# Kernel optimization log

Measured on AMD Instinct MI355X. Metric: run time of the kernel, lower is better.

## Reference

```python
import jax, jax.numpy as jnp
import numpy as np

D_MODEL = 1024
NUM_HEADS = 16
HEAD_DIM = D_MODEL // NUM_HEADS
B, S = 2, 2048


def setup_inputs() -> dict:
    key = jax.random.key(0)
    ks = jax.random.split(key, 16)
    sd = 1.0 / np.sqrt(D_MODEL)
    def lin(k):
        kw, kb = jax.random.split(k)
        W = jax.random.uniform(kw, (D_MODEL, D_MODEL), jnp.float32, -sd, sd)
        b = jax.random.uniform(kb, (D_MODEL,), jnp.float32, -sd, sd)
        return W, b
    Wq, bq = lin(ks[0]); Wk, bk = lin(ks[1]); Wv, bv = lin(ks[2]); Wo, bo = lin(ks[3])
    return {
        'q': jax.random.normal(ks[4], (B, S, D_MODEL), jnp.float32),
        'k': jax.random.normal(ks[5], (B, S, D_MODEL), jnp.float32),
        'v': jax.random.normal(ks[6], (B, S, D_MODEL), jnp.float32),
        'phase': jax.random.normal(ks[7], (B,), jnp.float32),
        'Wq': Wq, 'bq': bq, 'Wk': Wk, 'bk': bk, 'Wv': Wv, 'bv': bv, 'Wo': Wo, 'bo': bo,
        'phase_coupling': jnp.zeros((1, NUM_HEADS, 1, 1), jnp.float32),
        'attention_scale': jnp.ones((1,), jnp.float32),
        'stability_factor': jnp.ones((1,), jnp.float32),
    }


def reference(q, k, v, phase, Wq, bq, Wk, bk, Wv, bv, Wo, bo,
              phase_coupling, attention_scale, stability_factor):
    batch, seq, _ = q.shape
    scale = HEAD_DIM ** -0.5

    def split_heads(x):  # [B,S,D] -> [B,H,S,hd]
        return x.reshape(batch, -1, NUM_HEADS, HEAD_DIM).transpose(0, 2, 1, 3)

    qh = split_heads(q @ Wq.T + bq)
    kh = split_heads(k @ Wk.T + bk)
    vh = split_heads(v @ Wv.T + bv)

    scores = jnp.einsum('bhqd,bhkd->bhqk', qh, kh) * (scale * attention_scale)
    # phase modulation: phase [B] -> [B,1,1,1]; scores *= 1 + coupling*sin(phase)
    phase_factor = jnp.sin(phase)[:, None, None, None]
    scores = scores * (1.0 + phase_coupling * phase_factor)

    attn_weights = jax.nn.softmax(scores, axis=-1)  # dropout is identity in eval
    out = jnp.einsum('bhqk,bhkd->bhqd', attn_weights, vh)
    out = out.transpose(0, 2, 1, 3).reshape(batch, seq, D_MODEL)
    out = (out @ Wo.T + bo) * stability_factor
    return out, attn_weights
```

## Files before the change

kernel.cpp:

```cpp
#include <hip/hip_runtime.h>
#include <hip/hip_bf16.h>
#include <cstdint>
#include <cstddef>
#include <cmath>

#define NH 16
#define HD 64
#define SS 2048
#define DM 1024
#define MTOT 4096

typedef __attribute__((ext_vector_type(8))) short short8;
typedef __attribute__((ext_vector_type(4))) float float4v;
typedef __attribute__((ext_vector_type(4))) int int4v;
typedef __attribute__((ext_vector_type(4))) unsigned short ushort4v;

__device__ __forceinline__ unsigned short f2bf(float f){
  unsigned int u = __builtin_bit_cast(unsigned int, f);
  u += 0x7FFFu + ((u >> 16) & 1u);
  return (unsigned short)(u >> 16);
}

__device__ __forceinline__ void gload16(const void* g, void* l){
  __builtin_amdgcn_global_load_lds((const __attribute__((address_space(1))) void*)g,
                                   (__attribute__((address_space(3))) void*)l, 16, 0, 0);
}

__global__ __launch_bounds__(256) void cvt3_kernel(
    const float* __restrict__ s0, const float* __restrict__ s1, const float* __restrict__ s2,
    unsigned short* __restrict__ d0, unsigned short* __restrict__ d1, unsigned short* __restrict__ d2,
    int n){
  const int z = blockIdx.z;
  const float* src = z==0 ? s0 : (z==1 ? s1 : s2);
  unsigned short* dst = z==0 ? d0 : (z==1 ? d1 : d2);
  for (int i = (blockIdx.x*blockDim.x + threadIdx.x)*4; i < n; i += gridDim.x*blockDim.x*4){
    float4v v = *reinterpret_cast<const float4v*>(src + i);
    ushort4v o;
    o.x = f2bf(v.x); o.y = f2bf(v.y); o.z = f2bf(v.z); o.w = f2bf(v.w);
    *reinterpret_cast<ushort4v*>(dst + i) = o;
  }
}

__global__ __launch_bounds__(256) void cvt4_kernel(
    const float* __restrict__ s0, const float* __restrict__ s1,
    const float* __restrict__ s2, const float* __restrict__ s3,
    unsigned short* __restrict__ d0, unsigned short* __restrict__ d1,
    unsigned short* __restrict__ d2, unsigned short* __restrict__ d3,
    int n){
  const int z = blockIdx.z;
  const float* src = z==0 ? s0 : (z==1 ? s1 : (z==2 ? s2 : s3));
  unsigned short* dst = z==0 ? d0 : (z==1 ? d1 : (z==2 ? d2 : d3));
  for (int i = (blockIdx.x*blockDim.x + threadIdx.x)*4; i < n; i += gridDim.x*blockDim.x*4){
    float4v v = *reinterpret_cast<const float4v*>(src + i);
    ushort4v o;
    o.x = f2bf(v.x); o.y = f2bf(v.y); o.z = f2bf(v.z); o.w = f2bf(v.w);
    *reinterpret_cast<ushort4v*>(dst + i) = o;
  }
}

__global__ __launch_bounds__(256) void gemm_proj(
    const unsigned short* __restrict__ X0, const unsigned short* __restrict__ X1, const unsigned short* __restrict__ X2,
    const unsigned short* __restrict__ W0, const unsigned short* __restrict__ W1, const unsigned short* __restrict__ W2,
    const float* __restrict__ b0, const float* __restrict__ b1, const float* __restrict__ b2,
    unsigned short* __restrict__ O0, unsigned short* __restrict__ O1, unsigned short* __restrict__ O2){
  __shared__ unsigned short Alds[128*32];
  __shared__ unsigned short Blds[128*32];
  const int z = blockIdx.z;
  const unsigned short* A  = z==0 ? X0 : (z==1 ? X1 : X2);
  const unsigned short* Bw = z==0 ? W0 : (z==1 ? W1 : W2);
  const float* bias        = z==0 ? b0 : (z==1 ? b1 : b2);
  unsigned short* outp     = z==0 ? O0 : (z==1 ? O1 : O2);
  const bool vmode = (z == 2);
  const int K = DM;
  const int t = threadIdx.x;
  const int l = t & 63;
  const int w = t >> 6;
  const int m0 = blockIdx.y * 128, n0 = blockIdx.x * 128;
  const int wm = (w & 1)*64, wn = (w >> 1)*64;
  const int srow = t >> 2;
  const int scol = (t & 3)*8;
  const int lr = l & 15, lg = l >> 4;
  float4v acc[4][4] = {};
  for (int k0 = 0; k0 < K; k0 += 32){
    __syncthreads();
    gload16(A  + (size_t)(m0 + srow     )*K + k0 + scol, Alds + t*8);
    gload16(A  + (size_t)(m0 + srow + 64)*K + k0 + scol, Alds + 2048 + t*8);
    gload16(Bw + (size_t)(n0 + srow     )*K + k0 + scol, Blds + t*8);
    gload16(Bw + (size_t)(n0 + srow + 64)*K + k0 + scol, Blds + 2048 + t*8);
    asm volatile("s_waitcnt vmcnt(0)" ::: "memory");
    __syncthreads();
    short8 afrag[4], bfrag[4];
    #pragma unroll
    for (int mb = 0; mb < 4; ++mb)
      afrag[mb] = *reinterpret_cast<const short8*>(Alds + (wm + mb*16 + lr)*32 + lg*8);
    #pragma unroll
    for (int nb = 0; nb < 4; ++nb)
      bfrag[nb] = *reinterpret_cast<const short8*>(Blds + (wn + nb*16 + lr)*32 + lg*8);
    #pragma unroll
    for (int mb = 0; mb < 4; ++mb)
      #pragma unroll
      for (int nb = 0; nb < 4; ++nb)
        acc[mb][nb] = __builtin_amdgcn_mfma_f32_16x16x32_bf16(afrag[mb], bfrag[nb], acc[mb][nb], 0, 0, 0);
  }
  #pragma unroll
  for (int mb = 0; mb < 4; ++mb){
    #pragma unroll
    for (int nb = 0; nb < 4; ++nb){
      const int gn = n0 + wn + nb*16 + lr;
      const float biasv = bias[gn];
      #pragma unroll
      for (int r = 0; r < 4; ++r){
        const int gm = m0 + wm + mb*16 + lg*4 + r;
        float v = acc[mb][nb][r] + biasv;
        const int b_ = gm >> 11, s_ = gm & 2047, h_ = gn >> 6, d_ = gn & 63;
        if (!vmode)
          outp[((size_t)(b_*NH + h_)*SS + s_)*HD + d_] = f2bf(v);
        else
          outp[((size_t)(b_*NH + h_)*HD + d_)*SS + s_] = f2bf(v);
      }
    }
  }
}

__global__ __launch_bounds__(256) void gemm_out(const unsigned short* __restrict__ A,
                                                const unsigned short* __restrict__ Bw,
                                                const float* __restrict__ bias,
                                                float* __restrict__ outp,
                                                const float* __restrict__ oscale_p){
  __shared__ unsigned short Alds[128*32];
  __shared__ unsigned short Blds[128*32];
  const int K = DM, N = DM;
  const int t = threadIdx.x;
  const int l = t & 63;
  const int w = t >> 6;
  const int m0 = blockIdx.y * 128, n0 = blockIdx.x * 128;
  const int wm = (w & 1)*64, wn = (w >> 1)*64;
  const int srow = t >> 2;
  const int scol = (t & 3)*8;
  const int lr = l & 15, lg = l >> 4;
  float4v acc[4][4] = {};
  for (int k0 = 0; k0 < K; k0 += 32){
    __syncthreads();
    gload16(A  + (size_t)(m0 + srow     )*K + k0 + scol, Alds + t*8);
    gload16(A  + (size_t)(m0 + srow + 64)*K + k0 + scol, Alds + 2048 + t*8);
    gload16(Bw + (size_t)(n0 + srow     )*K + k0 + scol, Blds + t*8);
    gload16(Bw + (size_t)(n0 + srow + 64)*K + k0 + scol, Blds + 2048 + t*8);
    asm volatile("s_waitcnt vmcnt(0)" ::: "memory");
    __syncthreads();
    short8 afrag[4], bfrag[4];
    #pragma unroll
    for (int mb = 0; mb < 4; ++mb)
      afrag[mb] = *reinterpret_cast<const short8*>(Alds + (wm + mb*16 + lr)*32 + lg*8);
    #pragma unroll
    for (int nb = 0; nb < 4; ++nb)
      bfrag[nb] = *reinterpret_cast<const short8*>(Blds + (wn + nb*16 + lr)*32 + lg*8);
    #pragma unroll
    for (int mb = 0; mb < 4; ++mb)
      #pragma unroll
      for (int nb = 0; nb < 4; ++nb)
        acc[mb][nb] = __builtin_amdgcn_mfma_f32_16x16x32_bf16(afrag[mb], bfrag[nb], acc[mb][nb], 0, 0, 0);
  }
  const float osc = oscale_p[0];
  #pragma unroll
  for (int mb = 0; mb < 4; ++mb){
    #pragma unroll
    for (int nb = 0; nb < 4; ++nb){
      const int gn = n0 + wn + nb*16 + lr;
      const float biasv = bias[gn];
      #pragma unroll
      for (int r = 0; r < 4; ++r){
        const int gm = m0 + wm + mb*16 + lg*4 + r;
        outp[(size_t)gm*N + gn] = (acc[mb][nb][r] + biasv) * osc;
      }
    }
  }
}

__global__ __launch_bounds__(256, 4) void attn_kernel(
    const unsigned short* __restrict__ Qh,
    const unsigned short* __restrict__ Kh,
    const unsigned short* __restrict__ Vt,
    unsigned short* __restrict__ AO,
    float* __restrict__ attnW,
    const float* __restrict__ phase,
    const float* __restrict__ pc,
    const float* __restrict__ ascale)
{
  __shared__ float lred[4][32];
  __shared__ __attribute__((aligned(16))) float ored[4][32*32];

  const int t = threadIdx.x;
  const int w = t >> 6, l = t & 63;
  const int lr = l & 15, lg = l >> 4;
  const int bh = blockIdx.x, qt = blockIdx.y;
  const int b = bh >> 4, h = bh & 15;
  const int q0 = qt*32;
  const float scale2 = 0.125f * ascale[0] * (1.0f + pc[h] * sinf(phase[b]))
                       * 1.4426950408889634f;

  const unsigned short* qbase = Qh + ((size_t)bh*SS + q0 + lr)*HD + lg*8;
  short8 aq[2][2];
  aq[0][0] = *reinterpret_cast<const short8*>(qbase);
  aq[0][1] = *reinterpret_cast<const short8*>(qbase + 32);
  aq[1][0] = *reinterpret_cast<const short8*>(qbase + 16*HD);
  aq[1][1] = *reinterpret_cast<const short8*>(qbase + 16*HD + 32);

  const int tbase = w * 512;
  const unsigned short* kbase = Kh + ((size_t)bh*SS + tbase + lr)*HD + lg*8;

  float lsum[2] = {0.f, 0.f};
  #pragma unroll 2
  for (int tb = 0; tb < 32; ++tb){
    const unsigned short* kp = kbase + (size_t)tb*16*HD;
    short8 bk0 = *reinterpret_cast<const short8*>(kp);
    short8 bk1 = *reinterpret_cast<const short8*>(kp + 32);
    #pragma unroll
    for (int qs = 0; qs < 2; ++qs){
      float4v pacc = {};
      pacc = __builtin_amdgcn_mfma_f32_16x16x32_bf16(bk0, aq[qs][0], pacc, 0, 0, 0);
      pacc = __builtin_amdgcn_mfma_f32_16x16x32_bf16(bk1, aq[qs][1], pacc, 0, 0, 0);
      lsum[qs] += (exp2f(pacc[0]*scale2) + exp2f(pacc[1]*scale2))
                + (exp2f(pacc[2]*scale2) + exp2f(pacc[3]*scale2));
    }
  }
  #pragma unroll
  for (int mask = 16; mask < 64; mask <<= 1){
    lsum[0] += __shfl_xor(lsum[0], mask, 64);
    lsum[1] += __shfl_xor(lsum[1], mask, 64);
  }
  if (l < 16){
    lred[w][lr]    = lsum[0];
    lred[w][16+lr] = lsum[1];
  }
  __syncthreads();
  float cc[2];
  #pragma unroll
  for (int qs = 0; qs < 2; ++qs){
    const int row = qs*16 + lr;
    const float total = (lred[0][row] + lred[1][row]) + (lred[2][row] + lred[3][row]);
    cc[qs] = -__log2f(total);
  }

  float4v oacc[2][4] = {};
  float* gwq0 = attnW + ((size_t)bh*SS + q0 + lr)*SS + tbase;
  float* gwq1 = gwq0 + (size_t)16*SS;
  const unsigned short* vbase = Vt + ((size_t)bh*HD + lr)*SS + tbase + lg*8;
  const int idxA = (((lg & 1)*2)*16 + lr)*4;
  const int idxB = idxA + 64;
  const bool hi = (lg >= 2);

  short8 cA0 = *reinterpret_cast<const short8*>(kbase);
  short8 cA1 = *reinterpret_cast<const short8*>(kbase + 32);
  short8 cB0 = *reinterpret_cast<const short8*>(kbase + 16*HD);
  short8 cB1 = *reinterpret_cast<const short8*>(kbase + 16*HD + 32);
  short8 cv0 = *reinterpret_cast<const short8*>(vbase);
  short8 cv1 = *reinterpret_cast<const short8*>(vbase + (size_t)16*SS);
  short8 cv2 = *reinterpret_cast<const short8*>(vbase + (size_t)32*SS);
  short8 cv3 = *reinterpret_cast<const short8*>(vbase + (size_t)48*SS);

  #pragma unroll 2
  for (int tp = 0; tp < 16; ++tp){
    const int tn = (tp + 1) & 15;
    const unsigned short* kpn = kbase + (size_t)tn*32*HD;
    const short8 nA0 = *reinterpret_cast<const short8*>(kpn);
    const short8 nA1 = *reinterpret_cast<const short8*>(kpn + 32);
    const short8 nB0 = *reinterpret_cast<const short8*>(kpn + 16*HD);
    const short8 nB1 = *reinterpret_cast<const short8*>(kpn + 16*HD + 32);
    const short8 nv0 = *reinterpret_cast<const short8*>(vbase + tn*32);
    const short8 nv1 = *reinterpret_cast<const short8*>(vbase + (size_t)16*SS + tn*32);
    const short8 nv2 = *reinterpret_cast<const short8*>(vbase + (size_t)32*SS + tn*32);
    const short8 nv3 = *reinterpret_cast<const short8*>(vbase + (size_t)48*SS + tn*32);

    const int tloc = tp*32;
    #pragma unroll
    for (int qs = 0; qs < 2; ++qs){
      float4v pA = {};
      pA = __builtin_amdgcn_mfma_f32_16x16x32_bf16(cA0, aq[qs][0], pA, 0, 0, 0);
      pA = __builtin_amdgcn_mfma_f32_16x16x32_bf16(cA1, aq[qs][1], pA, 0, 0, 0);
      float4v pB = {};
      pB = __builtin_amdgcn_mfma_f32_16x16x32_bf16(cB0, aq[qs][0], pB, 0, 0, 0);
      pB = __builtin_amdgcn_mfma_f32_16x16x32_bf16(cB1, aq[qs][1], pB, 0, 0, 0);
      float4v eA, eB;
      eA.x = exp2f(fmaf(pA[0], scale2, cc[qs]));
      eA.y = exp2f(fmaf(pA[1], scale2, cc[qs]));
      eA.z = exp2f(fmaf(pA[2], scale2, cc[qs]));
      eA.w = exp2f(fmaf(pA[3], scale2, cc[qs]));
      eB.x = exp2f(fmaf(pB[0], scale2, cc[qs]));
      eB.y = exp2f(fmaf(pB[1], scale2, cc[qs]));
      eB.z = exp2f(fmaf(pB[2], scale2, cc[qs]));
      eB.w = exp2f(fmaf(pB[3], scale2, cc[qs]));
      const int w0A = ((int)f2bf(eA.y) << 16) | (int)f2bf(eA.x);
      const int w1A = ((int)f2bf(eA.w) << 16) | (int)f2bf(eA.z);
      const int w0B = ((int)f2bf(eB.y) << 16) | (int)f2bf(eB.x);
      const int w1B = ((int)f2bf(eB.w) << 16) | (int)f2bf(eB.z);

      const int a0 = __builtin_amdgcn_ds_bpermute(idxA, w0A);
      const int b0 = __builtin_amdgcn_ds_bpermute(idxA, w0B);
      const int a1 = __builtin_amdgcn_ds_bpermute(idxA, w1A);
      const int b1 = __builtin_amdgcn_ds_bpermute(idxA, w1B);
      const int a2 = __builtin_amdgcn_ds_bpermute(idxB, w0A);
      const int b2 = __builtin_amdgcn_ds_bpermute(idxB, w0B);
      const int a3 = __builtin_amdgcn_ds_bpermute(idxB, w1A);
      const int b3 = __builtin_amdgcn_ds_bpermute(idxB, w1B);
      int4v words;
      words.x = hi ? b0 : a0;
      words.y = hi ? b1 : a1;
      words.z = hi ? b2 : a2;
      words.w = hi ? b3 : a3;
      const short8 pa = __builtin_bit_cast(short8, words);

      oacc[qs][0] = __builtin_amdgcn_mfma_f32_16x16x32_bf16(pa, cv0, oacc[qs][0], 0, 0, 0);
      oacc[qs][1] = __builtin_amdgcn_mfma_f32_16x16x32_bf16(pa, cv1, oacc[qs][1], 0, 0, 0);
      oacc[qs][2] = __builtin_amdgcn_mfma_f32_16x16x32_bf16(pa, cv2, oacc[qs][2], 0, 0, 0);
      oacc[qs][3] = __builtin_amdgcn_mfma_f32_16x16x32_bf16(pa, cv3, oacc[qs][3], 0, 0, 0);

      float* gw = qs ? gwq1 : gwq0;
      __builtin_nontemporal_store(eA, reinterpret_cast<float4v*>(gw + tloc + lg*4));
      __builtin_nontemporal_store(eB, reinterpret_cast<float4v*>(gw + tloc + 16 + lg*4));
    }

    cA0 = nA0; cA1 = nA1; cB0 = nB0; cB1 = nB1;
    cv0 = nv0; cv1 = nv1; cv2 = nv2; cv3 = nv3;
  }

  #pragma unroll
  for (int c = 0; c < 2; ++c){
    if (c) __syncthreads();
    #pragma unroll
    for (int qs = 0; qs < 2; ++qs)
      #pragma unroll
      for (int dl = 0; dl < 2; ++dl)
        #pragma unroll
        for (int r = 0; r < 4; ++r)
          ored[w][(qs*16 + lg*4 + r)*32 + dl*16 + lr] = oacc[qs][c*2 + dl][r];
    __syncthreads();
    const int row = t >> 3, c4 = (t & 7);
    const float4v* o0 = reinterpret_cast<const float4v*>(&ored[0][0]);
    const int fi = row*8 + c4;
    float4v s = o0[fi];
    s += o0[fi + 256];
    s += o0[fi + 512];
    s += o0[fi + 768];
    ushort4v o4;
    o4.x = f2bf(s.x); o4.y = f2bf(s.y); o4.z = f2bf(s.z); o4.w = f2bf(s.w);
    *reinterpret_cast<ushort4v*>(AO + ((size_t)b*SS + q0 + row)*DM + h*HD + c*32 + c4*4) = o4;
  }
}

extern "C" void kernel_launch(void* const* d_in, const int* in_sizes, int n_in,
                              void* d_out, int out_size, void* d_ws, size_t ws_size,
                              hipStream_t stream){
  const float* q      = (const float*)d_in[0];
  const float* k      = (const float*)d_in[1];
  const float* v      = (const float*)d_in[2];
  const float* phase  = (const float*)d_in[3];
  const float* Wq     = (const float*)d_in[4];
  const float* bq     = (const float*)d_in[5];
  const float* Wk     = (const float*)d_in[6];
  const float* bk     = (const float*)d_in[7];
  const float* Wv     = (const float*)d_in[8];
  const float* bv     = (const float*)d_in[9];
  const float* Wo     = (const float*)d_in[10];
  const float* bo     = (const float*)d_in[11];
  const float* pc     = (const float*)d_in[12];
  const float* ascale = (const float*)d_in[13];
  const float* stab   = (const float*)d_in[14];

  unsigned short* Xq  = (unsigned short*)d_ws;
  unsigned short* Xk  = Xq  + 4194304;
  unsigned short* Xv  = Xk  + 4194304;
  unsigned short* Wqb = Xv  + 4194304;
  unsigned short* Wkb = Wqb + 1048576;
  unsigned short* Wvb = Wkb + 1048576;
  unsigned short* Wob = Wvb + 1048576;
  unsigned short* Qh  = Wob + 1048576;
  unsigned short* Kh  = Qh  + 4194304;
  unsigned short* Vt  = Kh  + 4194304;
  unsigned short* AO  = Vt  + 4194304;

  float* out0  = (float*)d_out;
  float* attnW = out0 + (size_t)MTOT*DM;

  cvt3_kernel<<<dim3(512,1,3), 256, 0, stream>>>(q, k, v, Xq, Xk, Xv, MTOT*DM);
  cvt4_kernel<<<dim3(128,1,4), 256, 0, stream>>>(Wq, Wk, Wv, Wo, Wqb, Wkb, Wvb, Wob, DM*DM);

  gemm_proj<<<dim3(DM/128, MTOT/128, 3), 256, 0, stream>>>(
      Xq, Xk, Xv, Wqb, Wkb, Wvb, bq, bk, bv, Qh, Kh, Vt);

  attn_kernel<<<dim3(32, SS/32, 1), 256, 0, stream>>>(Qh, Kh, Vt, AO, attnW,
                                                      phase, pc, ascale);

  gemm_out<<<dim3(DM/128, MTOT/128, 1), 256, 0, stream>>>(AO, Wob, bo, out0, stab);
}
```

Baseline: 310.3 us.

## Stage attention-weight tiles in LDS for coalesced full-row global stores

The second pass of the attention kernel now walks the keys in chunks of 256, with the four waves interleaved inside each chunk. The exp-normalized weights are written to a padded shared-memory tile and then stored to the attention-weight output as contiguous 1 KB row segments, replacing the scattered 16-byte nontemporal stores. The aim is better write coalescing for the large fp32 attention-weight output. The cost is two block barriers per chunk, extra LDS traffic and a larger shared footprint (about 33 KB), and the register prefetch of the next K/V tiles has been removed.

```diff
diff --git a/kernel.cpp b/kernel.cpp
--- a/kernel.cpp
+++ b/kernel.cpp
@@ -187,7 +187,7 @@
     const float* __restrict__ ascale)
 {
   __shared__ float lred[4][32];
-  __shared__ __attribute__((aligned(16))) float ored[4][32*32];
+  __shared__ __attribute__((aligned(16))) float smem[32*260];
 
   const int t = threadIdx.x;
   const int w = t >> 6, l = t & 63;
@@ -205,13 +205,11 @@
   aq[1][0] = *reinterpret_cast<const short8*>(qbase + 16*HD);
   aq[1][1] = *reinterpret_cast<const short8*>(qbase + 16*HD + 32);
 
-  const int tbase = w * 512;
-  const unsigned short* kbase = Kh + ((size_t)bh*SS + tbase + lr)*HD + lg*8;
-
+  const unsigned short* kbase1 = Kh + ((size_t)bh*SS + w*512 + lr)*HD + lg*8;
   float lsum[2] = {0.f, 0.f};
   #pragma unroll 2
   for (int tb = 0; tb < 32; ++tb){
-    const unsigned short* kp = kbase + (size_t)tb*16*HD;
+    const unsigned short* kp = kbase1 + (size_t)tb*16*HD;
     short8 bk0 = *reinterpret_cast<const short8*>(kp);
     short8 bk1 = *reinterpret_cast<const short8*>(kp + 32);
     #pragma unroll
@@ -242,87 +240,84 @@
   }
 
   float4v oacc[2][4] = {};
-  float* gwq0 = attnW + ((size_t)bh*SS + q0 + lr)*SS + tbase;
-  float* gwq1 = gwq0 + (size_t)16*SS;
-  const unsigned short* vbase = Vt + ((size_t)bh*HD + lr)*SS + tbase + lg*8;
+  float* gwb = attnW + ((size_t)bh*SS + q0)*SS;
+  const unsigned short* kb2 = Kh + ((size_t)bh*SS + lr)*HD + lg*8;
+  const unsigned short* vb2 = Vt + ((size_t)bh*HD + lr)*SS + lg*8;
   const int idxA = (((lg & 1)*2)*16 + lr)*4;
   const int idxB = idxA + 64;
   const bool hi = (lg >= 2);
 
-  short8 cA0 = *reinterpret_cast<const short8*>(kbase);
-  short8 cA1 = *reinterpret_cast<const short8*>(kbase + 32);
-  short8 cB0 = *reinterpret_cast<const short8*>(kbase + 16*HD);
-  short8 cB1 = *reinterpret_cast<const short8*>(kbase + 16*HD + 32);
-  short8 cv0 = *reinterpret_cast<const short8*>(vbase);
-  short8 cv1 = *reinterpret_cast<const short8*>(vbase + (size_t)16*SS);
-  short8 cv2 = *reinterpret_cast<const short8*>(vbase + (size_t)32*SS);
-  short8 cv3 = *reinterpret_cast<const short8*>(vbase + (size_t)48*SS);
-
-  #pragma unroll 2
-  for (int tp = 0; tp < 16; ++tp){
-    const int tn = (tp + 1) & 15;
-    const unsigned short* kpn = kbase + (size_t)tn*32*HD;
-    const short8 nA0 = *reinterpret_cast<const short8*>(kpn);
-    const short8 nA1 = *reinterpret_cast<const short8*>(kpn + 32);
-    const short8 nB0 = *reinterpret_cast<const short8*>(kpn + 16*HD);
-    const short8 nB1 = *reinterpret_cast<const short8*>(kpn + 16*HD + 32);
-    const short8 nv0 = *reinterpret_cast<const short8*>(vbase + tn*32);
-    const short8 nv1 = *reinterpret_cast<const short8*>(vbase + (size_t)16*SS + tn*32);
-    const short8 nv2 = *reinterpret_cast<const short8*>(vbase + (size_t)32*SS + tn*32);
-    const short8 nv3 = *reinterpret_cast<const short8*>(vbase + (size_t)48*SS + tn*32);
-
-    const int tloc = tp*32;
-    #pragma unroll
-    for (int qs = 0; qs < 2; ++qs){
-      float4v pA = {};
-      pA = __builtin_amdgcn_mfma_f32_16x16x32_bf16(cA0, aq[qs][0], pA, 0, 0, 0);
-      pA = __builtin_amdgcn_mfma_f32_16x16x32_bf16(cA1, aq[qs][1], pA, 0, 0, 0);
-      float4v pB = {};
-      pB = __builtin_amdgcn_mfma_f32_16x16x32_bf16(cB0, aq[qs][0], pB, 0, 0, 0);
-      pB = __builtin_amdgcn_mfma_f32_16x16x32_bf16(cB1, aq[qs][1], pB, 0, 0, 0);
-      float4v eA, eB;
-      eA.x = exp2f(fmaf(pA[0], scale2, cc[qs]));
-      eA.y = exp2f(fmaf(pA[1], scale2, cc[qs]));
-      eA.z = exp2f(fmaf(pA[2], scale2, cc[qs]));
-      eA.w = exp2f(fmaf(pA[3], scale2, cc[qs]));
-      eB.x = exp2f(fmaf(pB[0], scale2, cc[qs]));
-      eB.y = exp2f(fmaf(pB[1], scale2, cc[qs]));
-      eB.z = exp2f(fmaf(pB[2], scale2, cc[qs]));
-      eB.w = exp2f(fmaf(pB[3], scale2, cc[qs]));
-      const int w0A = ((int)f2bf(eA.y) << 16) | (int)f2bf(eA.x);
-      const int w1A = ((int)f2bf(eA.w) << 16) | (int)f2bf(eA.z);
-      const int w0B = ((int)f2bf(eB.y) << 16) | (int)f2bf(eB.x);
-      const int w1B = ((int)f2bf(eB.w) << 16) | (int)f2bf(eB.z);
-
-      const int a0 = __builtin_amdgcn_ds_bpermute(idxA, w0A);
-      const int b0 = __builtin_amdgcn_ds_bpermute(idxA, w0B);
-      const int a1 = __builtin_amdgcn_ds_bpermute(idxA, w1A);
-      const int b1 = __builtin_amdgcn_ds_bpermute(idxA, w1B);
-      const int a2 = __builtin_amdgcn_ds_bpermute(idxB, w0A);
-      const int b2 = __builtin_amdgcn_ds_bpermute(idxB, w0B);
-      const int a3 = __builtin_amdgcn_ds_bpermute(idxB, w1A);
-      const int b3 = __builtin_amdgcn_ds_bpermute(idxB, w1B);
-      int4v words;
-      words.x = hi ? b0 : a0;
-      words.y = hi ? b1 : a1;
-      words.z = hi ? b2 : a2;
-      words.w = hi ? b3 : a3;
-      const short8 pa = __builtin_bit_cast(short8, words);
-
-      oacc[qs][0] = __builtin_amdgcn_mfma_f32_16x16x32_bf16(pa, cv0, oacc[qs][0], 0, 0, 0);
-      oacc[qs][1] = __builtin_amdgcn_mfma_f32_16x16x32_bf16(pa, cv1, oacc[qs][1], 0, 0, 0);
-      oacc[qs][2] = __builtin_amdgcn_mfma_f32_16x16x32_bf16(pa, cv2, oacc[qs][2], 0, 0, 0);
-      oacc[qs][3] = __builtin_amdgcn_mfma_f32_16x16x32_bf16(pa, cv3, oacc[qs][3], 0, 0, 0);
-
-      float* gw = qs ? gwq1 : gwq0;
-      __builtin_nontemporal_store(eA, reinterpret_cast<float4v*>(gw + tloc + lg*4));
-      __builtin_nontemporal_store(eB, reinterpret_cast<float4v*>(gw + tloc + 16 + lg*4));
-    }
-
-    cA0 = nA0; cA1 = nA1; cB0 = nB0; cB1 = nB1;
-    cv0 = nv0; cv1 = nv1; cv2 = nv2; cv3 = nv3;
-  }
-
+  for (int ch = 0; ch < 8; ++ch){
+    #pragma unroll
+    for (int sub = 0; sub < 2; ++sub){
+      const int tloc = ch*256 + w*64 + sub*32;
+      const unsigned short* kp = kb2 + (size_t)tloc*HD;
+      short8 k0A = *reinterpret_cast<const short8*>(kp);
+      short8 k1A = *reinterpret_cast<const short8*>(kp + 32);
+      short8 k0B = *reinterpret_cast<const short8*>(kp + 16*HD);
+      short8 k1B = *reinterpret_cast<const short8*>(kp + 16*HD + 32);
+      short8 bv[4];
+      #pragma unroll
+      for (int dt = 0; dt < 4; ++dt)
+        bv[dt] = *reinterpret_cast<const short8*>(vb2 + (size_t)(dt*16)*SS + tloc);
+
+      #pragma unroll
+      for (int qs = 0; qs < 2; ++qs){
+        float4v pA = {};
+        pA = __builtin_amdgcn_mfma_f32_16x16x32_bf16(k0A, aq[qs][0], pA, 0, 0, 0);
+        pA = __builtin_amdgcn_mfma_f32_16x16x32_bf16(k1A, aq[qs][1], pA, 0, 0, 0);
+        float4v pB = {};
+        pB = __builtin_amdgcn_mfma_f32_16x16x32_bf16(k0B, aq[qs][0], pB, 0, 0, 0);
+        pB = __builtin_amdgcn_mfma_f32_16x16x32_bf16(k1B, aq[qs][1], pB, 0, 0, 0);
+        float4v eA, eB;
+        eA.x = exp2f(fmaf(pA[0], scale2, cc[qs]));
+        eA.y = exp2f(fmaf(pA[1], scale2, cc[qs]));
+        eA.z = exp2f(fmaf(pA[2], scale2, cc[qs]));
+        eA.w = exp2f(fmaf(pA[3], scale2, cc[qs]));
+        eB.x = exp2f(fmaf(pB[0], scale2, cc[qs]));
+        eB.y = exp2f(fmaf(pB[1], scale2, cc[qs]));
+        eB.z = exp2f(fmaf(pB[2], scale2, cc[qs]));
+        eB.w = exp2f(fmaf(pB[3], scale2, cc[qs]));
+
+        const int cw = w*64 + sub*32;
+        *reinterpret_cast<float4v*>(&smem[(qs*16 + lr)*260 + cw + lg*4]) = eA;
+        *reinterpret_cast<float4v*>(&smem[(qs*16 + lr)*260 + cw + 16 + lg*4]) = eB;
+
+        const int w0A = ((int)f2bf(eA.y) << 16) | (int)f2bf(eA.x);
+        const int w1A = ((int)f2bf(eA.w) << 16) | (int)f2bf(eA.z);
+        const int w0B = ((int)f2bf(eB.y) << 16) | (int)f2bf(eB.x);
+        const int w1B = ((int)f2bf(eB.w) << 16) | (int)f2bf(eB.z);
+        const int a0 = __builtin_amdgcn_ds_bpermute(idxA, w0A);
+        const int b0 = __builtin_amdgcn_ds_bpermute(idxA, w0B);
+        const int a1 = __builtin_amdgcn_ds_bpermute(idxA, w1A);
+        const int b1 = __builtin_amdgcn_ds_bpermute(idxA, w1B);
+        const int a2 = __builtin_amdgcn_ds_bpermute(idxB, w0A);
+        const int b2 = __builtin_amdgcn_ds_bpermute(idxB, w0B);
+        const int a3 = __builtin_amdgcn_ds_bpermute(idxB, w1A);
+        const int b3 = __builtin_amdgcn_ds_bpermute(idxB, w1B);
+        int4v words;
+        words.x = hi ? b0 : a0;
+        words.y = hi ? b1 : a1;
+        words.z = hi ? b2 : a2;
+        words.w = hi ? b3 : a3;
+        const short8 pa = __builtin_bit_cast(short8, words);
+        #pragma unroll
+        for (int dt = 0; dt < 4; ++dt)
+          oacc[qs][dt] = __builtin_amdgcn_mfma_f32_16x16x32_bf16(pa, bv[dt], oacc[qs][dt], 0, 0, 0);
+      }
+    }
+    __syncthreads();
+    #pragma unroll
+    for (int i = 0; i < 8; ++i){
+      const int row = i*4 + w;
+      const float4v val = *reinterpret_cast<const float4v*>(&smem[row*260 + l*4]);
+      __builtin_nontemporal_store(val,
+        reinterpret_cast<float4v*>(gwb + (size_t)row*SS + ch*256 + l*4));
+    }
+    __syncthreads();
+  }
+
+  float* ored = smem;
   #pragma unroll
   for (int c = 0; c < 2; ++c){
     if (c) __syncthreads();
@@ -332,10 +327,10 @@
       for (int dl = 0; dl < 2; ++dl)
         #pragma unroll
         for (int r = 0; r < 4; ++r)
-          ored[w][(qs*16 + lg*4 + r)*32 + dl*16 + lr] = oacc[qs][c*2 + dl][r];
+          ored[w*1024 + (qs*16 + lg*4 + r)*32 + dl*16 + lr] = oacc[qs][c*2 + dl][r];
     __syncthreads();
     const int row = t >> 3, c4 = (t & 7);
-    const float4v* o0 = reinterpret_cast<const float4v*>(&ored[0][0]);
+    const float4v* o0 = reinterpret_cast<const float4v*>(smem);
     const int fi = row*8 + c4;
     float4v s = o0[fi];
     s += o0[fi + 256];
```

Measured after the change: 288.9 us (median of 2 runs). 1.07x faster.
